# Performance work log

Hardware: AMD Instinct MI355X
Metric: run time of the kernel (lower is better)

## Reference

```python
import jax, jax.numpy as jnp
import numpy as np

B, N, C, H = 8, 1024, 1024, 16
D = C // H
SCALE = D ** -0.5


def setup_inputs() -> dict:
    key = jax.random.key(0)
    ks = jax.random.split(key, 5)
    s = 0.02  # keep pre-softmax logits in a sane range
    return {
        "x": jax.random.normal(ks[0], (B, N, C), dtype=jnp.float32),
        "Wq": jax.random.normal(ks[1], (C, C), dtype=jnp.float32) * s,
        "bq": jax.random.normal(ks[2], (C,), dtype=jnp.float32) * s,
        "Wkv": jax.random.normal(ks[3], (C, 2 * C), dtype=jnp.float32) * s,
        "bkv": jax.random.normal(ks[4], (2 * C,), dtype=jnp.float32) * s,
    }


def reference(x, Wq, bq, Wkv, bkv):
    b, n, c = x.shape
    h, d = H, c // H
    q = (x @ Wq + bq).reshape(b, n, h, d)                 # [b,n,h,d]
    kv = x @ Wkv + bkv                                     # [b,n,2c]
    k, v = jnp.split(kv, 2, axis=-1)                       # each [b,n,c]
    k = k.reshape(b, n, h, d)
    v = v.reshape(b, n, h, d)
    att = jnp.einsum("bnhd,bmhd->bnmh", q, k) * SCALE      # [b,n,m,h]
    att = jax.nn.softmax(att, axis=2)                      # softmax over keys (m)
    out = jnp.einsum("bnmh,bmhd->bnhd", att, v).reshape(b, n, c)
    return out
```

## Files before the change

kernel.cpp:

```cpp
#include <hip/hip_runtime.h>
#include <stdint.h>

using u16 = unsigned short;
using u32 = unsigned int;
using bf16x8 = __attribute__((ext_vector_type(8))) __bf16;
using f32x4  = __attribute__((ext_vector_type(4))) float;

#define NB 8
#define NN 1024
#define NC 1024
#define NH 16
#define ND 64
#define QSCALE 0.18033688011112042f

__device__ __forceinline__ u16 f2bf(float f) {
  u32 u = __float_as_uint(f);
  return (u16)((u + 0x7fffu + ((u >> 16) & 1u)) >> 16);
}
__device__ __forceinline__ u16 bfc(float f) {
  __bf16 b = (__bf16)f;
  return __builtin_bit_cast(u16, b);
}
__device__ __forceinline__ u32 pack2(u16 a, u16 b) { return (u32)a | ((u32)b << 16); }

__device__ __forceinline__ void gload16(const void* g, void* l) {
  __builtin_amdgcn_global_load_lds((__attribute__((address_space(1))) const u32*)g,
                                   (__attribute__((address_space(3))) u32*)l, 16, 0, 0);
}

__global__ void k_cvt_x(const float* __restrict__ x, u16* __restrict__ xb, int n4) {
  int i = blockIdx.x * blockDim.x + threadIdx.x;
  if (i >= n4) return;
  float4 v = ((const float4*)x)[i];
  ((uint2*)xb)[i] = make_uint2(pack2(f2bf(v.x), f2bf(v.y)), pack2(f2bf(v.z), f2bf(v.w)));
}

__global__ void k_prep_w(const float* __restrict__ Wq, const float* __restrict__ Wkv,
                         u16* __restrict__ Wt) {
  __shared__ u16 tile[64][72];
  int k0 = blockIdx.x * 64;
  int c0 = blockIdx.y * 64;
  int t  = threadIdx.x;
  bool isQ = (c0 < 1024);
  const float* src = isQ ? Wq : Wkv;
  int ldw  = isQ ? 1024 : 2048;
  int csrc = isQ ? c0 : (c0 - 1024);
  float sc = isQ ? QSCALE : 1.0f;

  int r  = t >> 2;
  int cq = (t & 3) << 4;
  const float* p = src + (size_t)(k0 + r) * ldw + csrc + cq;
#pragma unroll
  for (int j = 0; j < 16; j += 4) {
    float4 v = *(const float4*)(p + j);
    tile[r][cq + j + 0] = f2bf(v.x * sc);
    tile[r][cq + j + 1] = f2bf(v.y * sc);
    tile[r][cq + j + 2] = f2bf(v.z * sc);
    tile[r][cq + j + 3] = f2bf(v.w * sc);
  }
  __syncthreads();
  int co = t >> 2;
  int kq = (t & 3) << 4;
  u16 v0[16];
#pragma unroll
  for (int j = 0; j < 16; ++j) v0[j] = tile[kq + j][co];
  uint4 o0, o1;
  o0.x = pack2(v0[0], v0[1]);  o0.y = pack2(v0[2], v0[3]);
  o0.z = pack2(v0[4], v0[5]);  o0.w = pack2(v0[6], v0[7]);
  o1.x = pack2(v0[8], v0[9]);  o1.y = pack2(v0[10], v0[11]);
  o1.z = pack2(v0[12], v0[13]); o1.w = pack2(v0[14], v0[15]);
  u16* dst = Wt + (size_t)(c0 + co) * 1024 + k0 + kq;
  *(uint4*)dst = o0;
  *(uint4*)(dst + 8) = o1;
}

__global__ void k_bias(const float* __restrict__ bq, const float* __restrict__ bkv,
                       float* __restrict__ bias) {
  int i = blockIdx.x * 256 + threadIdx.x;
  if (i < 1024) bias[i] = bq[i] * QSCALE;
  else if (i < 3072) bias[i] = bkv[i - 1024];
}

__launch_bounds__(256)
__global__ void k_gemm(const u16* __restrict__ A, const u16* __restrict__ Bw,
                       const float* __restrict__ bias,
                       u16* __restrict__ qws, u16* __restrict__ kws, u16* __restrict__ vws) {
  __shared__ __align__(16) u16 As[128 * 32];
  __shared__ __align__(16) u16 Bs[128 * 32];
  int m0 = blockIdx.x * 128;
  int n0 = blockIdx.y * 128;
  int tid = threadIdx.x;
  int wave = tid >> 6, lane = tid & 63;
  int lo = lane & 15, hi = lane >> 4;
  int wr = wave >> 1, wc = wave & 1;

  f32x4 acc[4][4] = {};

  const u16* gA = A  + (size_t)(m0 + (wave * 2) * 16 + (lane >> 2)) * 1024 + (lane & 3) * 8;
  const u16* gB = Bw + (size_t)(n0 + (wave * 2) * 16 + (lane >> 2)) * 1024 + (lane & 3) * 8;
  u16* lA = As + (wave * 2) * 512;
  u16* lB = Bs + (wave * 2) * 512;

  for (int ko = 0; ko < 1024; ko += 32) {
    gload16(gA + ko,             lA);
    gload16(gA + ko + 16 * 1024, lA + 512);
    gload16(gB + ko,             lB);
    gload16(gB + ko + 16 * 1024, lB + 512);
    __syncthreads();
    bf16x8 af[4], bv[4];
#pragma unroll
    for (int mi = 0; mi < 4; ++mi)
      af[mi] = *(const bf16x8*)(As + (wr * 64 + mi * 16 + lo) * 32 + hi * 8);
#pragma unroll
    for (int ni = 0; ni < 4; ++ni)
      bv[ni] = *(const bf16x8*)(Bs + (wc * 64 + ni * 16 + lo) * 32 + hi * 8);
#pragma unroll
    for (int mi = 0; mi < 4; ++mi)
#pragma unroll
      for (int ni = 0; ni < 4; ++ni)
        acc[mi][ni] = __builtin_amdgcn_mfma_f32_16x16x32_bf16(af[mi], bv[ni], acc[mi][ni], 0, 0, 0);
    __syncthreads();
  }

#pragma unroll
  for (int ni = 0; ni < 4; ++ni) {
    int c = n0 + wc * 64 + ni * 16 + lo;
    float bvl = bias[c];
#pragma unroll
    for (int mi = 0; mi < 4; ++mi) {
#pragma unroll
      for (int r = 0; r < 4; ++r) {
        int m = m0 + wr * 64 + mi * 16 + hi * 4 + r;
        int b = m >> 10, tok = m & 1023;
        u16 o = f2bf(acc[mi][ni][r] + bvl);
        if (c < 1024) {
          int h = c >> 6, d = c & 63;
          qws[((size_t)(b * 16 + h) * 1024 + tok) * 64 + d] = o;
        } else if (c < 2048) {
          int c2 = c - 1024; int h = c2 >> 6, d = c2 & 63;
          kws[((size_t)(b * 16 + h) * 1024 + tok) * 64 + d] = o;
        } else {
          int c2 = c - 2048; int h = c2 >> 6, d = c2 & 63;
          vws[((size_t)(b * 16 + h) * 1024 + tok) * 64 + d] = o;
        }
      }
    }
  }
}

__global__ void k_tr_v(const u16* __restrict__ v, u16* __restrict__ vt) {
  __shared__ u16 t[64][72];
  int n0 = blockIdx.x * 64;
  int bh = blockIdx.y;
  int tid = threadIdx.x;
  const u16* src = v + ((size_t)bh * 1024 + n0) * 64;
#pragma unroll
  for (int p = 0; p < 2; ++p) {
    int r = p * 32 + (tid >> 3);
    int c = (tid & 7) * 8;
    *(uint4*)&t[r][c] = *(const uint4*)(src + r * 64 + c);
  }
  __syncthreads();
  int d = tid >> 2;
  int nq = (tid & 3) * 16;
  u16 v0[16];
#pragma unroll
  for (int j = 0; j < 16; ++j) v0[j] = t[nq + j][d];
  uint4 o0, o1;
  o0.x = pack2(v0[0], v0[1]);  o0.y = pack2(v0[2], v0[3]);
  o0.z = pack2(v0[4], v0[5]);  o0.w = pack2(v0[6], v0[7]);
  o1.x = pack2(v0[8], v0[9]);  o1.y = pack2(v0[10], v0[11]);
  o1.z = pack2(v0[12], v0[13]); o1.w = pack2(v0[14], v0[15]);
  u16* dst = vt + ((size_t)bh * 64 + d) * 1024 + n0 + nq;
  *(uint4*)dst = o0;
  *(uint4*)(dst + 8) = o1;
}

__launch_bounds__(512)
__global__ void k_attn(const u16* __restrict__ q, const u16* __restrict__ k,
                       const u16* __restrict__ vt, float* __restrict__ out) {
  __shared__ __align__(16) u16 Ks[2][4096];
  __shared__ __align__(16) u16 Vs[2][4096];
  __shared__ __align__(16) u16 P[8][16][72];
  int bh = blockIdx.x;
  int q0 = blockIdx.y * 128;
  int tid = threadIdx.x;
  int w = tid >> 6, lane = tid & 63;
  int lo = lane & 15, hi = lane >> 4;
  int b = bh >> 4, h = bh & 15;

  const u16* kbase = k  + (size_t)bh * 65536;
  const u16* vbase = vt + (size_t)bh * 65536;

  int srow = w * 8 + (lane >> 3);
  int cg   = (lane & 7) ^ ((lane >> 3) & 7);
  const u16* gK = kbase + (size_t)srow * 64   + cg * 8;
  const u16* gV = vbase + (size_t)srow * 1024 + cg * 8;
  u16* lK0 = &Ks[0][w * 512];
  u16* lK1 = &Ks[1][w * 512];
  u16* lV0 = &Vs[0][w * 512];
  u16* lV1 = &Vs[1][w * 512];

  const u16* qp = q + ((size_t)bh * 1024 + q0 + w * 16 + lo) * 64 + hi * 8;
  bf16x8 qf0 = *(const bf16x8*)(qp);
  bf16x8 qf1 = *(const bf16x8*)(qp + 32);

  f32x4 acc_o[4] = {};
  float m_s = -1e30f;
  float l_s = 0.f;

  int sw = lo & 7;

  gload16(gK, lK0);
  gload16(gV, lV0);
  __syncthreads();

  for (int t = 0; t < 16; ++t) {
    int cur = t & 1;
    if (t < 15) {
      gload16(gK + (t + 1) * 4096, cur ? lK0 : lK1);
      gload16(gV + (t + 1) * 64,   cur ? lV0 : lV1);
    }
    f32x4 s[4] = {};
    const u16* kb = Ks[cur];
#pragma unroll
    for (int ni = 0; ni < 4; ++ni) {
      const u16* kp = kb + (ni * 16 + lo) * 64;
      bf16x8 kf0 = *(const bf16x8*)(kp + ((hi ^ sw) * 8));
      bf16x8 kf1 = *(const bf16x8*)(kp + (((4 + hi) ^ sw) * 8));
      s[ni] = __builtin_amdgcn_mfma_f32_16x16x32_bf16(kf0, qf0, s[ni], 0, 0, 0);
      s[ni] = __builtin_amdgcn_mfma_f32_16x16x32_bf16(kf1, qf1, s[ni], 0, 0, 0);
    }
    float pm;
    {
      float a0 = fmaxf(fmaxf(s[0][0], s[0][1]), fmaxf(s[0][2], s[0][3]));
      float a1 = fmaxf(fmaxf(s[1][0], s[1][1]), fmaxf(s[1][2], s[1][3]));
      float a2 = fmaxf(fmaxf(s[2][0], s[2][1]), fmaxf(s[2][2], s[2][3]));
      float a3 = fmaxf(fmaxf(s[3][0], s[3][1]), fmaxf(s[3][2], s[3][3]));
      pm = fmaxf(fmaxf(a0, a1), fmaxf(a2, a3));
      pm = fmaxf(pm, __shfl_xor(pm, 16));
      pm = fmaxf(pm, __shfl_xor(pm, 32));
    }
    if (!__all(pm <= m_s + 8.0f)) {
      float mn = fmaxf(m_s, pm);
      float corr = __builtin_amdgcn_exp2f(m_s - mn);
      m_s = mn;
      l_s *= corr;
      float cr[4];
#pragma unroll
      for (int r = 0; r < 4; ++r) cr[r] = __shfl(corr, hi * 4 + r);
#pragma unroll
      for (int ci = 0; ci < 4; ++ci)
#pragma unroll
        for (int r = 0; r < 4; ++r) acc_o[ci][r] *= cr[r];
    }
    float rs = 0.f;
#pragma unroll
    for (int ni = 0; ni < 4; ++ni) {
      float p0 = __builtin_amdgcn_exp2f(s[ni][0] - m_s);
      float p1 = __builtin_amdgcn_exp2f(s[ni][1] - m_s);
      float p2 = __builtin_amdgcn_exp2f(s[ni][2] - m_s);
      float p3 = __builtin_amdgcn_exp2f(s[ni][3] - m_s);
      rs += (p0 + p1) + (p2 + p3);
      ushort4 pk;
      pk.x = bfc(p0); pk.y = bfc(p1); pk.z = bfc(p2); pk.w = bfc(p3);
      *(ushort4*)&P[w][lo][ni * 16 + hi * 4] = pk;
    }
    rs += __shfl_xor(rs, 16);
    rs += __shfl_xor(rs, 32);
    l_s += rs;
    bf16x8 pf0 = *(const bf16x8*)(&P[w][lo][hi * 8]);
    bf16x8 pf1 = *(const bf16x8*)(&P[w][lo][32 + hi * 8]);
    const u16* vb = Vs[cur];
#pragma unroll
    for (int ci = 0; ci < 4; ++ci) {
      const u16* vp = vb + (ci * 16 + lo) * 64;
      bf16x8 vf0 = *(const bf16x8*)(vp + ((hi ^ sw) * 8));
      bf16x8 vf1 = *(const bf16x8*)(vp + (((4 + hi) ^ sw) * 8));
      acc_o[ci] = __builtin_amdgcn_mfma_f32_16x16x32_bf16(pf0, vf0, acc_o[ci], 0, 0, 0);
      acc_o[ci] = __builtin_amdgcn_mfma_f32_16x16x32_bf16(pf1, vf1, acc_o[ci], 0, 0, 0);
    }
    __syncthreads();
  }
  float inv = 1.0f / l_s;
  float ivr[4];
#pragma unroll
  for (int r = 0; r < 4; ++r) ivr[r] = __shfl(inv, hi * 4 + r);
#pragma unroll
  for (int r = 0; r < 4; ++r) {
    int n = q0 + w * 16 + hi * 4 + r;
    float* dst = out + ((size_t)(b * 1024 + n)) * 1024 + h * 64;
#pragma unroll
    for (int ci = 0; ci < 4; ++ci) dst[ci * 16 + lo] = acc_o[ci][r] * ivr[r];
  }
}

extern "C" void kernel_launch(void* const* d_in, const int* in_sizes, int n_in,
                              void* d_out, int out_size, void* d_ws, size_t ws_size,
                              hipStream_t stream) {
  const float* x   = (const float*)d_in[0];
  const float* Wq  = (const float*)d_in[1];
  const float* bq  = (const float*)d_in[2];
  const float* Wkv = (const float*)d_in[3];
  const float* bkv = (const float*)d_in[4];
  float* out = (float*)d_out;

  char* ws = (char*)d_ws;
  u16*   xb   = (u16*)(ws);
  u16*   Wt   = (u16*)(ws + 16777216);
  float* bias = (float*)(ws + 23068672);
  u16*   qws  = (u16*)(ws + 23080960);
  u16*   kws  = (u16*)(ws + 39858176);
  u16*   vws  = (u16*)(ws + 56635392);
  u16*   vtw  = (u16*)(ws + 73412608);

  k_cvt_x<<<8192, 256, 0, stream>>>(x, xb, 2097152);
  {
    dim3 g(16, 48);
    k_prep_w<<<g, 256, 0, stream>>>(Wq, Wkv, Wt);
  }
  k_bias<<<12, 256, 0, stream>>>(bq, bkv, bias);
  {
    dim3 g(64, 24);
    k_gemm<<<g, 256, 0, stream>>>(xb, Wt, bias, qws, kws, vws);
  }
  {
    dim3 g(16, 128);
    k_tr_v<<<g, 256, 0, stream>>>(vws, vtw);
  }
  {
    dim3 g(128, 8);
    k_attn<<<g, 512, 0, stream>>>(qws, kws, vtw, out);
  }
}
```

Baseline: 148.9 us.

## Rewrite projection GEMM with 256x256 tiles, double-buffered swizzled LDS and interleaved prefetch

The QKV projection GEMM moves from 128x128 tiles with 4 waves and a single LDS buffer to 256x256 tiles with 8 waves, BK=64, and double-buffered LDS. The LDS layout is XOR-swizzled to avoid bank conflicts, and the global loads for the next k-step are split and interleaved between MFMA quadrants, with barriers and setprio to overlap memory and compute. The goals are higher arithmetic intensity per block and hidden load latency. In exchange it uses 128KB of LDS per block and a large accumulator register footprint, and the grid drops to 384 blocks, which may leave CUs underfilled.

```diff
diff --git a/kernel.cpp b/kernel.cpp
--- a/kernel.cpp
+++ b/kernel.cpp
@@ -81,58 +81,117 @@
   else if (i < 3072) bias[i] = bkv[i - 1024];
 }
 
-__launch_bounds__(256)
+__launch_bounds__(512, 2)
 __global__ void k_gemm(const u16* __restrict__ A, const u16* __restrict__ Bw,
                        const float* __restrict__ bias,
                        u16* __restrict__ qws, u16* __restrict__ kws, u16* __restrict__ vws) {
-  __shared__ __align__(16) u16 As[128 * 32];
-  __shared__ __align__(16) u16 Bs[128 * 32];
-  int m0 = blockIdx.x * 128;
-  int n0 = blockIdx.y * 128;
+  __shared__ __align__(16) u16 Ab[2][16384];
+  __shared__ __align__(16) u16 Bb[2][16384];
+  int m0 = blockIdx.x * 256;
+  int n0 = blockIdx.y * 256;
   int tid = threadIdx.x;
-  int wave = tid >> 6, lane = tid & 63;
+  int w = tid >> 6, lane = tid & 63;
   int lo = lane & 15, hi = lane >> 4;
-  int wr = wave >> 1, wc = wave & 1;
-
-  f32x4 acc[4][4] = {};
-
-  const u16* gA = A  + (size_t)(m0 + (wave * 2) * 16 + (lane >> 2)) * 1024 + (lane & 3) * 8;
-  const u16* gB = Bw + (size_t)(n0 + (wave * 2) * 16 + (lane >> 2)) * 1024 + (lane & 3) * 8;
-  u16* lA = As + (wave * 2) * 512;
-  u16* lB = Bs + (wave * 2) * 512;
-
-  for (int ko = 0; ko < 1024; ko += 32) {
-    gload16(gA + ko,             lA);
-    gload16(gA + ko + 16 * 1024, lA + 512);
-    gload16(gB + ko,             lB);
-    gload16(gB + ko + 16 * 1024, lB + 512);
-    __syncthreads();
-    bf16x8 af[4], bv[4];
-#pragma unroll
-    for (int mi = 0; mi < 4; ++mi)
-      af[mi] = *(const bf16x8*)(As + (wr * 64 + mi * 16 + lo) * 32 + hi * 8);
-#pragma unroll
-    for (int ni = 0; ni < 4; ++ni)
-      bv[ni] = *(const bf16x8*)(Bs + (wc * 64 + ni * 16 + lo) * 32 + hi * 8);
-#pragma unroll
-    for (int mi = 0; mi < 4; ++mi)
-#pragma unroll
-      for (int ni = 0; ni < 4; ++ni)
-        acc[mi][ni] = __builtin_amdgcn_mfma_f32_16x16x32_bf16(af[mi], bv[ni], acc[mi][ni], 0, 0, 0);
-    __syncthreads();
-  }
-
-#pragma unroll
-  for (int ni = 0; ni < 4; ++ni) {
-    int c = n0 + wc * 64 + ni * 16 + lo;
+  int wm = w >> 2, wn = w & 3;
+
+  f32x4 acc[8][4] = {};
+
+  int srow8 = lane >> 3;
+  int cs = (lane & 7) ^ srow8;
+  const u16* Ag = A  + (size_t)(m0 + w * 16 + srow8) * 1024 + cs * 8;
+  const u16* Bg = Bw + (size_t)(n0 + w * 16 + srow8) * 1024 + cs * 8;
+  int w2 = w * 2;
+
+  int sw = lo & 7;
+  int ck0 = ((hi) ^ sw) * 8;
+  int ck1 = ((4 + hi) ^ sw) * 8;
+  int arow = wm * 128 + lo;
+  int brow = wn * 64 + lo;
+
+#define STAGE4(gp, lp)                                        \
+  gload16((gp),                (lp) + w2 * 512);              \
+  gload16((gp) + 8 * 1024,     (lp) + (w2 + 1) * 512);        \
+  gload16((gp) + 128 * 1024,   (lp) + 8192 + w2 * 512);       \
+  gload16((gp) + 136 * 1024,   (lp) + 8192 + (w2 + 1) * 512);
+
+#define BARRIER() __builtin_amdgcn_s_barrier(); __builtin_amdgcn_sched_barrier(0)
+
+#define QUAD(AH, NH, AF)                                                          \
+  __builtin_amdgcn_s_setprio(1);                                                  \
+  _Pragma("unroll")                                                               \
+  for (int ks = 0; ks < 2; ++ks)                                                  \
+    _Pragma("unroll")                                                             \
+    for (int mi = 0; mi < 4; ++mi)                                                \
+      _Pragma("unroll")                                                           \
+      for (int ni = 0; ni < 2; ++ni)                                              \
+        acc[(AH) * 4 + mi][(NH) * 2 + ni] = __builtin_amdgcn_mfma_f32_16x16x32_bf16( \
+            AF[mi][ks], bf[NH][ni][ks], acc[(AH) * 4 + mi][(NH) * 2 + ni], 0, 0, 0); \
+  __builtin_amdgcn_s_setprio(0);
+
+  STAGE4(Ag, Ab[0]);
+  STAGE4(Bg, Bb[0]);
+  asm volatile("s_waitcnt vmcnt(0)" ::: "memory");
+  BARRIER();
+
+  for (int t = 0; t < 16; ++t) {
+    const u16* Acur = Ab[t & 1];
+    const u16* Bcur = Bb[t & 1];
+    u16* An = Ab[(t & 1) ^ 1];
+    u16* Bn = Bb[(t & 1) ^ 1];
+    int kn = (t + 1) * 64;
+    bool pre = (t < 15);
+
+    bf16x8 a0f[4][2], a1f[4][2], bf[2][2][2];
+#pragma unroll
+    for (int mi = 0; mi < 4; ++mi) {
+      const u16* p = Acur + (arow + mi * 16) * 64;
+      a0f[mi][0] = *(const bf16x8*)(p + ck0);
+      a0f[mi][1] = *(const bf16x8*)(p + ck1);
+    }
+#pragma unroll
+    for (int nh = 0; nh < 2; ++nh)
+#pragma unroll
+      for (int ni = 0; ni < 2; ++ni) {
+        const u16* p = Bcur + (brow + nh * 32 + ni * 16) * 64;
+        bf[nh][ni][0] = *(const bf16x8*)(p + ck0);
+        bf[nh][ni][1] = *(const bf16x8*)(p + ck1);
+      }
+    if (pre) { STAGE4(Ag + kn, An); }
+    BARRIER();
+    QUAD(0, 0, a0f);
+    BARRIER();
+    if (pre) { STAGE4(Bg + kn, Bn); }
+    BARRIER();
+    QUAD(0, 1, a0f);
+    BARRIER();
+#pragma unroll
+    for (int mi = 0; mi < 4; ++mi) {
+      const u16* p = Acur + (arow + 64 + mi * 16) * 64;
+      a1f[mi][0] = *(const bf16x8*)(p + ck0);
+      a1f[mi][1] = *(const bf16x8*)(p + ck1);
+    }
+    BARRIER();
+    QUAD(1, 0, a1f);
+    BARRIER();
+    QUAD(1, 1, a1f);
+    asm volatile("s_waitcnt vmcnt(0)" ::: "memory");
+    BARRIER();
+  }
+#undef STAGE4
+#undef BARRIER
+#undef QUAD
+
+#pragma unroll
+  for (int ni4 = 0; ni4 < 4; ++ni4) {
+    int c = n0 + wn * 64 + ni4 * 16 + lo;
     float bvl = bias[c];
 #pragma unroll
-    for (int mi = 0; mi < 4; ++mi) {
+    for (int mi8 = 0; mi8 < 8; ++mi8) {
 #pragma unroll
       for (int r = 0; r < 4; ++r) {
-        int m = m0 + wr * 64 + mi * 16 + hi * 4 + r;
+        int m = m0 + wm * 128 + mi8 * 16 + hi * 4 + r;
         int b = m >> 10, tok = m & 1023;
-        u16 o = f2bf(acc[mi][ni][r] + bvl);
+        u16 o = f2bf(acc[mi8][ni4][r] + bvl);
         if (c < 1024) {
           int h = c >> 6, d = c & 63;
           qws[((size_t)(b * 16 + h) * 1024 + tok) * 64 + d] = o;
@@ -321,8 +380,8 @@
   }
   k_bias<<<12, 256, 0, stream>>>(bq, bkv, bias);
   {
-    dim3 g(64, 24);
-    k_gemm<<<g, 256, 0, stream>>>(xb, Wt, bias, qws, kws, vws);
+    dim3 g(32, 12);
+    k_gemm<<<g, 512, 0, stream>>>(xb, Wt, bias, qws, kws, vws);
   }
   {
     dim3 g(16, 128);
```

Result: no change. 148.5 us (-0.3%).

## Enlarge QKV GEMM tiles and add 4-stage async LDS pipeline with swizzle

Applied to the files above, without the earlier changes.

The projection GEMM moves from 128x128 tiles with 256 threads to 256x256 tiles with 512 threads. It adds a four-buffer LDS ring where global-to-LDS loads run two stages ahead, using vmcnt waits with a single barrier per k-step instead of two. The LDS layout is XOR-swizzled to avoid bank conflicts. This targets the load-latency stalls and sync overhead of the single-buffered loop, at the cost of 128KB of LDS, more accumulator registers and only 384 blocks across the grid.

```diff
diff --git a/kernel.cpp b/kernel.cpp
--- a/kernel.cpp
+++ b/kernel.cpp
@@ -81,56 +81,86 @@
   else if (i < 3072) bias[i] = bkv[i - 1024];
 }
 
-__launch_bounds__(256)
+__launch_bounds__(512, 2)
 __global__ void k_gemm(const u16* __restrict__ A, const u16* __restrict__ Bw,
                        const float* __restrict__ bias,
                        u16* __restrict__ qws, u16* __restrict__ kws, u16* __restrict__ vws) {
-  __shared__ __align__(16) u16 As[128 * 32];
-  __shared__ __align__(16) u16 Bs[128 * 32];
-  int m0 = blockIdx.x * 128;
-  int n0 = blockIdx.y * 128;
+  __shared__ __align__(16) u16 RA[4][8192];
+  __shared__ __align__(16) u16 RB[4][8192];
+  int m0 = blockIdx.x * 256;
+  int n0 = blockIdx.y * 256;
   int tid = threadIdx.x;
-  int wave = tid >> 6, lane = tid & 63;
+  int w = tid >> 6, lane = tid & 63;
   int lo = lane & 15, hi = lane >> 4;
-  int wr = wave >> 1, wc = wave & 1;
-
-  f32x4 acc[4][4] = {};
-
-  const u16* gA = A  + (size_t)(m0 + (wave * 2) * 16 + (lane >> 2)) * 1024 + (lane & 3) * 8;
-  const u16* gB = Bw + (size_t)(n0 + (wave * 2) * 16 + (lane >> 2)) * 1024 + (lane & 3) * 8;
-  u16* lA = As + (wave * 2) * 512;
-  u16* lB = Bs + (wave * 2) * 512;
-
-  for (int ko = 0; ko < 1024; ko += 32) {
-    gload16(gA + ko,             lA);
-    gload16(gA + ko + 16 * 1024, lA + 512);
-    gload16(gB + ko,             lB);
-    gload16(gB + ko + 16 * 1024, lB + 512);
-    __syncthreads();
-    bf16x8 af[4], bv[4];
-#pragma unroll
-    for (int mi = 0; mi < 4; ++mi)
-      af[mi] = *(const bf16x8*)(As + (wr * 64 + mi * 16 + lo) * 32 + hi * 8);
-#pragma unroll
-    for (int ni = 0; ni < 4; ++ni)
-      bv[ni] = *(const bf16x8*)(Bs + (wc * 64 + ni * 16 + lo) * 32 + hi * 8);
-#pragma unroll
-    for (int mi = 0; mi < 4; ++mi)
-#pragma unroll
-      for (int ni = 0; ni < 4; ++ni)
-        acc[mi][ni] = __builtin_amdgcn_mfma_f32_16x16x32_bf16(af[mi], bv[ni], acc[mi][ni], 0, 0, 0);
-    __syncthreads();
-  }
+  int wm = w >> 2, wn = w & 3;
+
+  f32x4 acc[8][4] = {};
+
+  int srow = w * 16 + (lane >> 2);
+  int csw  = ((lane & 3) ^ ((lane >> 3) & 3)) * 8;
+  const u16* Ag = A  + (size_t)(m0 + srow) * 1024 + csw;
+  const u16* Bg = Bw + (size_t)(n0 + srow) * 1024 + csw;
+  int ldsoff = w * 512;
+
+  int ck = ((hi ^ ((lo >> 1) & 3)) << 3);
+  int arow = (wm * 128 + lo) * 32;
+  int brow = (wn * 64 + lo) * 32;
+
+#define STAGEU(U)                                                   \
+  {                                                                 \
+    int _s = (U) & 3;                                               \
+    const u16* _ag = Ag + (U) * 32;                                 \
+    const u16* _bg = Bg + (U) * 32;                                 \
+    gload16(_ag,              &RA[_s][ldsoff]);                     \
+    gload16(_ag + 128 * 1024, &RA[_s][4096 + ldsoff]);              \
+    gload16(_bg,              &RB[_s][ldsoff]);                     \
+    gload16(_bg + 128 * 1024, &RB[_s][4096 + ldsoff]);              \
+  }
+
+#define COMPUTEU(U)                                                 \
+  {                                                                 \
+    int _s = (U) & 3;                                               \
+    bf16x8 af[8], bfr[4];                                           \
+    _Pragma("unroll")                                               \
+    for (int mi = 0; mi < 8; ++mi)                                  \
+      af[mi] = *(const bf16x8*)(&RA[_s][arow + mi * 512 + ck]);     \
+    _Pragma("unroll")                                               \
+    for (int ni = 0; ni < 4; ++ni)                                  \
+      bfr[ni] = *(const bf16x8*)(&RB[_s][brow + ni * 512 + ck]);    \
+    _Pragma("unroll")                                               \
+    for (int mi = 0; mi < 8; ++mi)                                  \
+      _Pragma("unroll")                                             \
+      for (int ni = 0; ni < 4; ++ni)                                \
+        acc[mi][ni] = __builtin_amdgcn_mfma_f32_16x16x32_bf16(      \
+            af[mi], bfr[ni], acc[mi][ni], 0, 0, 0);                 \
+  }
+
+  STAGEU(0);
+  STAGEU(1);
+  for (int u = 0; u < 30; ++u) {
+    STAGEU(u + 2);
+    asm volatile("s_waitcnt vmcnt(8)" ::: "memory");
+    __builtin_amdgcn_s_barrier();
+    COMPUTEU(u);
+  }
+  asm volatile("s_waitcnt vmcnt(4)" ::: "memory");
+  __builtin_amdgcn_s_barrier();
+  COMPUTEU(30);
+  asm volatile("s_waitcnt vmcnt(0)" ::: "memory");
+  __builtin_amdgcn_s_barrier();
+  COMPUTEU(31);
+#undef STAGEU
+#undef COMPUTEU
 
 #pragma unroll
   for (int ni = 0; ni < 4; ++ni) {
-    int c = n0 + wc * 64 + ni * 16 + lo;
+    int c = n0 + wn * 64 + ni * 16 + lo;
     float bvl = bias[c];
 #pragma unroll
-    for (int mi = 0; mi < 4; ++mi) {
+    for (int mi = 0; mi < 8; ++mi) {
 #pragma unroll
       for (int r = 0; r < 4; ++r) {
-        int m = m0 + wr * 64 + mi * 16 + hi * 4 + r;
+        int m = m0 + wm * 128 + mi * 16 + hi * 4 + r;
         int b = m >> 10, tok = m & 1023;
         u16 o = f2bf(acc[mi][ni][r] + bvl);
         if (c < 1024) {
@@ -321,8 +351,8 @@
   }
   k_bias<<<12, 256, 0, stream>>>(bq, bkv, bias);
   {
-    dim3 g(64, 24);
-    k_gemm<<<g, 256, 0, stream>>>(xb, Wt, bias, qws, kws, vws);
+    dim3 g(32, 12);
+    k_gemm<<<g, 512, 0, stream>>>(xb, Wt, bias, qws, kws, vws);
   }
   {
     dim3 g(16, 128);
```

Measured after the change: 144.6 us. 1.03x faster.

## Merge prep kernels, fuse V transpose into double-buffered swizzled GEMM epilogue

Applied to the files above, without the earlier changes.

Merges the x-conversion, weight-transpose and bias kernels into one launch. The QKV GEMM now uses 512 threads with a 128x256 tile, double-buffered LDS staging with an XOR swizzle, and an L2-friendly block remap. V is written straight out in transposed layout from the GEMM epilogue, which removes the separate transpose kernel and the intermediate V buffer. The trade-offs are more LDS per block and strided 8-byte transposed stores for V.

```diff
diff --git a/kernel.cpp b/kernel.cpp
--- a/kernel.cpp
+++ b/kernel.cpp
@@ -28,152 +28,151 @@
                                    (__attribute__((address_space(3))) u32*)l, 16, 0, 0);
 }
 
-__global__ void k_cvt_x(const float* __restrict__ x, u16* __restrict__ xb, int n4) {
-  int i = blockIdx.x * blockDim.x + threadIdx.x;
-  if (i >= n4) return;
-  float4 v = ((const float4*)x)[i];
-  ((uint2*)xb)[i] = make_uint2(pack2(f2bf(v.x), f2bf(v.y)), pack2(f2bf(v.z), f2bf(v.w)));
-}
-
-__global__ void k_prep_w(const float* __restrict__ Wq, const float* __restrict__ Wkv,
-                         u16* __restrict__ Wt) {
+__global__ void k_prep(const float* __restrict__ x, const float* __restrict__ Wq,
+                       const float* __restrict__ bq, const float* __restrict__ Wkv,
+                       const float* __restrict__ bkv,
+                       u16* __restrict__ xb, u16* __restrict__ Wt, float* __restrict__ bias) {
   __shared__ u16 tile[64][72];
-  int k0 = blockIdx.x * 64;
-  int c0 = blockIdx.y * 64;
-  int t  = threadIdx.x;
-  bool isQ = (c0 < 1024);
-  const float* src = isQ ? Wq : Wkv;
-  int ldw  = isQ ? 1024 : 2048;
-  int csrc = isQ ? c0 : (c0 - 1024);
-  float sc = isQ ? QSCALE : 1.0f;
-
-  int r  = t >> 2;
-  int cq = (t & 3) << 4;
-  const float* p = src + (size_t)(k0 + r) * ldw + csrc + cq;
-#pragma unroll
-  for (int j = 0; j < 16; j += 4) {
-    float4 v = *(const float4*)(p + j);
-    tile[r][cq + j + 0] = f2bf(v.x * sc);
-    tile[r][cq + j + 1] = f2bf(v.y * sc);
-    tile[r][cq + j + 2] = f2bf(v.z * sc);
-    tile[r][cq + j + 3] = f2bf(v.w * sc);
-  }
-  __syncthreads();
-  int co = t >> 2;
-  int kq = (t & 3) << 4;
-  u16 v0[16];
-#pragma unroll
-  for (int j = 0; j < 16; ++j) v0[j] = tile[kq + j][co];
-  uint4 o0, o1;
-  o0.x = pack2(v0[0], v0[1]);  o0.y = pack2(v0[2], v0[3]);
-  o0.z = pack2(v0[4], v0[5]);  o0.w = pack2(v0[6], v0[7]);
-  o1.x = pack2(v0[8], v0[9]);  o1.y = pack2(v0[10], v0[11]);
-  o1.z = pack2(v0[12], v0[13]); o1.w = pack2(v0[14], v0[15]);
-  u16* dst = Wt + (size_t)(c0 + co) * 1024 + k0 + kq;
-  *(uint4*)dst = o0;
-  *(uint4*)(dst + 8) = o1;
-}
-
-__global__ void k_bias(const float* __restrict__ bq, const float* __restrict__ bkv,
-                       float* __restrict__ bias) {
-  int i = blockIdx.x * 256 + threadIdx.x;
-  if (i < 1024) bias[i] = bq[i] * QSCALE;
-  else if (i < 3072) bias[i] = bkv[i - 1024];
-}
-
-__launch_bounds__(256)
+  int bid = blockIdx.x;
+  int t = threadIdx.x;
+  if (bid < 8192) {
+    int i = bid * 256 + t;
+    float4 v = ((const float4*)x)[i];
+    ((uint2*)xb)[i] = make_uint2(pack2(f2bf(v.x), f2bf(v.y)), pack2(f2bf(v.z), f2bf(v.w)));
+    return;
+  }
+  if (bid < 8960) {
+    int pb = bid - 8192;
+    int k0 = (pb & 15) << 6;
+    int c0 = (pb >> 4) << 6;
+    bool isQ = (c0 < 1024);
+    const float* src = isQ ? Wq : Wkv;
+    int ldw  = isQ ? 1024 : 2048;
+    int csrc = isQ ? c0 : (c0 - 1024);
+    float sc = isQ ? QSCALE : 1.0f;
+
+    int r  = t >> 2;
+    int cq = (t & 3) << 4;
+    const float* p = src + (size_t)(k0 + r) * ldw + csrc + cq;
+#pragma unroll
+    for (int j = 0; j < 16; j += 4) {
+      float4 v = *(const float4*)(p + j);
+      tile[r][cq + j + 0] = f2bf(v.x * sc);
+      tile[r][cq + j + 1] = f2bf(v.y * sc);
+      tile[r][cq + j + 2] = f2bf(v.z * sc);
+      tile[r][cq + j + 3] = f2bf(v.w * sc);
+    }
+    __syncthreads();
+    int co = t >> 2;
+    int kq = (t & 3) << 4;
+    u16 v0[16];
+#pragma unroll
+    for (int j = 0; j < 16; ++j) v0[j] = tile[kq + j][co];
+    uint4 o0, o1;
+    o0.x = pack2(v0[0], v0[1]);  o0.y = pack2(v0[2], v0[3]);
+    o0.z = pack2(v0[4], v0[5]);  o0.w = pack2(v0[6], v0[7]);
+    o1.x = pack2(v0[8], v0[9]);  o1.y = pack2(v0[10], v0[11]);
+    o1.z = pack2(v0[12], v0[13]); o1.w = pack2(v0[14], v0[15]);
+    u16* dst = Wt + (size_t)(c0 + co) * 1024 + k0 + kq;
+    *(uint4*)dst = o0;
+    *(uint4*)(dst + 8) = o1;
+    return;
+  }
+  {
+    int i = (bid - 8960) * 256 + t;
+    if (i < 1024) bias[i] = bq[i] * QSCALE;
+    else if (i < 3072) bias[i] = bkv[i - 1024];
+  }
+}
+
+__launch_bounds__(512, 4)
 __global__ void k_gemm(const u16* __restrict__ A, const u16* __restrict__ Bw,
                        const float* __restrict__ bias,
-                       u16* __restrict__ qws, u16* __restrict__ kws, u16* __restrict__ vws) {
-  __shared__ __align__(16) u16 As[128 * 32];
-  __shared__ __align__(16) u16 Bs[128 * 32];
-  int m0 = blockIdx.x * 128;
-  int n0 = blockIdx.y * 128;
+                       u16* __restrict__ qws, u16* __restrict__ kws, u16* __restrict__ vtw) {
+  __shared__ __align__(16) u16 Ab[2][4096];
+  __shared__ __align__(16) u16 Bb[2][8192];
+  int flat = blockIdx.x;
+  int swz = (flat & 7) * 96 + (flat >> 3);
+  int m0 = (swz & 63) * 128;
+  int n0 = (swz >> 6) * 256;
   int tid = threadIdx.x;
-  int wave = tid >> 6, lane = tid & 63;
+  int w = tid >> 6, lane = tid & 63;
   int lo = lane & 15, hi = lane >> 4;
-  int wr = wave >> 1, wc = wave & 1;
+  int wm = w >> 2, wn = w & 3;
 
   f32x4 acc[4][4] = {};
 
-  const u16* gA = A  + (size_t)(m0 + (wave * 2) * 16 + (lane >> 2)) * 1024 + (lane & 3) * 8;
-  const u16* gB = Bw + (size_t)(n0 + (wave * 2) * 16 + (lane >> 2)) * 1024 + (lane & 3) * 8;
-  u16* lA = As + (wave * 2) * 512;
-  u16* lB = Bs + (wave * 2) * 512;
-
-  for (int ko = 0; ko < 1024; ko += 32) {
-    gload16(gA + ko,             lA);
-    gload16(gA + ko + 16 * 1024, lA + 512);
-    gload16(gB + ko,             lB);
-    gload16(gB + ko + 16 * 1024, lB + 512);
+  int srow = tid >> 2;
+  int schunk = (tid & 3) ^ ((tid >> 3) & 3);
+  const u16* Ag  = A  + (size_t)(m0 + srow) * 1024 + schunk * 8;
+  const u16* Bg0 = Bw + (size_t)(n0 + srow) * 1024 + schunk * 8;
+  const u16* Bg1 = Bw + (size_t)(n0 + 128 + srow) * 1024 + schunk * 8;
+
+  int ck = ((hi ^ ((lo >> 1) & 3)) << 3);
+
+#define STAGE(BUF, KO)                                  \
+  gload16(Ag  + (KO), &Ab[BUF][tid * 8]);               \
+  gload16(Bg0 + (KO), &Bb[BUF][tid * 8]);               \
+  gload16(Bg1 + (KO), &Bb[BUF][4096 + tid * 8]);
+
+  STAGE(0, 0);
+  __syncthreads();
+
+  for (int t = 0; t < 32; ++t) {
+    int cb = t & 1;
+    if (t < 31) { STAGE(cb ^ 1, (t + 1) * 32); }
+    bf16x8 af[4], bfr[4];
+#pragma unroll
+    for (int mi = 0; mi < 4; ++mi)
+      af[mi] = *(const bf16x8*)&Ab[cb][(wm * 64 + mi * 16 + lo) * 32 + ck];
+#pragma unroll
+    for (int ni = 0; ni < 4; ++ni)
+      bfr[ni] = *(const bf16x8*)&Bb[cb][(wn * 64 + ni * 16 + lo) * 32 + ck];
+#pragma unroll
+    for (int mi = 0; mi < 4; ++mi)
+#pragma unroll
+      for (int ni = 0; ni < 4; ++ni)
+        acc[mi][ni] = __builtin_amdgcn_mfma_f32_16x16x32_bf16(af[mi], bfr[ni], acc[mi][ni], 0, 0, 0);
     __syncthreads();
-    bf16x8 af[4], bv[4];
-#pragma unroll
-    for (int mi = 0; mi < 4; ++mi)
-      af[mi] = *(const bf16x8*)(As + (wr * 64 + mi * 16 + lo) * 32 + hi * 8);
-#pragma unroll
-    for (int ni = 0; ni < 4; ++ni)
-      bv[ni] = *(const bf16x8*)(Bs + (wc * 64 + ni * 16 + lo) * 32 + hi * 8);
-#pragma unroll
-    for (int mi = 0; mi < 4; ++mi)
-#pragma unroll
-      for (int ni = 0; ni < 4; ++ni)
-        acc[mi][ni] = __builtin_amdgcn_mfma_f32_16x16x32_bf16(af[mi], bv[ni], acc[mi][ni], 0, 0, 0);
-    __syncthreads();
-  }
+  }
+#undef STAGE
 
 #pragma unroll
   for (int ni = 0; ni < 4; ++ni) {
-    int c = n0 + wc * 64 + ni * 16 + lo;
+    int c = n0 + wn * 64 + ni * 16 + lo;
     float bvl = bias[c];
-#pragma unroll
-    for (int mi = 0; mi < 4; ++mi) {
-#pragma unroll
-      for (int r = 0; r < 4; ++r) {
-        int m = m0 + wr * 64 + mi * 16 + hi * 4 + r;
-        int b = m >> 10, tok = m & 1023;
-        u16 o = f2bf(acc[mi][ni][r] + bvl);
-        if (c < 1024) {
-          int h = c >> 6, d = c & 63;
-          qws[((size_t)(b * 16 + h) * 1024 + tok) * 64 + d] = o;
-        } else if (c < 2048) {
-          int c2 = c - 1024; int h = c2 >> 6, d = c2 & 63;
-          kws[((size_t)(b * 16 + h) * 1024 + tok) * 64 + d] = o;
-        } else {
-          int c2 = c - 2048; int h = c2 >> 6, d = c2 & 63;
-          vws[((size_t)(b * 16 + h) * 1024 + tok) * 64 + d] = o;
+    if (c < 2048) {
+#pragma unroll
+      for (int mi = 0; mi < 4; ++mi) {
+#pragma unroll
+        for (int r = 0; r < 4; ++r) {
+          int m = m0 + wm * 64 + mi * 16 + hi * 4 + r;
+          int b = m >> 10, tok = m & 1023;
+          u16 o = f2bf(acc[mi][ni][r] + bvl);
+          if (c < 1024) {
+            int h = c >> 6, d = c & 63;
+            qws[((size_t)(b * 16 + h) * 1024 + tok) * 64 + d] = o;
+          } else {
+            int c2 = c - 1024; int h = c2 >> 6, d = c2 & 63;
+            kws[((size_t)(b * 16 + h) * 1024 + tok) * 64 + d] = o;
+          }
         }
       }
-    }
-  }
-}
-
-__global__ void k_tr_v(const u16* __restrict__ v, u16* __restrict__ vt) {
-  __shared__ u16 t[64][72];
-  int n0 = blockIdx.x * 64;
-  int bh = blockIdx.y;
-  int tid = threadIdx.x;
-  const u16* src = v + ((size_t)bh * 1024 + n0) * 64;
-#pragma unroll
-  for (int p = 0; p < 2; ++p) {
-    int r = p * 32 + (tid >> 3);
-    int c = (tid & 7) * 8;
-    *(uint4*)&t[r][c] = *(const uint4*)(src + r * 64 + c);
-  }
-  __syncthreads();
-  int d = tid >> 2;
-  int nq = (tid & 3) * 16;
-  u16 v0[16];
-#pragma unroll
-  for (int j = 0; j < 16; ++j) v0[j] = t[nq + j][d];
-  uint4 o0, o1;
-  o0.x = pack2(v0[0], v0[1]);  o0.y = pack2(v0[2], v0[3]);
-  o0.z = pack2(v0[4], v0[5]);  o0.w = pack2(v0[6], v0[7]);
-  o1.x = pack2(v0[8], v0[9]);  o1.y = pack2(v0[10], v0[11]);
-  o1.z = pack2(v0[12], v0[13]); o1.w = pack2(v0[14], v0[15]);
-  u16* dst = vt + ((size_t)bh * 64 + d) * 1024 + n0 + nq;
-  *(uint4*)dst = o0;
-  *(uint4*)(dst + 8) = o1;
+    } else {
+      int c2 = c - 2048; int h = c2 >> 6, d = c2 & 63;
+#pragma unroll
+      for (int mi = 0; mi < 4; ++mi) {
+        int m = m0 + wm * 64 + mi * 16 + hi * 4;
+        int b = m >> 10, tok = m & 1023;
+        ushort4 pk;
+        pk.x = bfc(acc[mi][ni][0] + bvl);
+        pk.y = bfc(acc[mi][ni][1] + bvl);
+        pk.z = bfc(acc[mi][ni][2] + bvl);
+        pk.w = bfc(acc[mi][ni][3] + bvl);
+        *(ushort4*)&vtw[((size_t)(b * 16 + h) * 64 + d) * 1024 + tok] = pk;
+      }
+    }
+  }
 }
 
 __launch_bounds__(512)
@@ -311,23 +310,10 @@
   float* bias = (float*)(ws + 23068672);
   u16*   qws  = (u16*)(ws + 23080960);
   u16*   kws  = (u16*)(ws + 39858176);
-  u16*   vws  = (u16*)(ws + 56635392);
   u16*   vtw  = (u16*)(ws + 73412608);
 
-  k_cvt_x<<<8192, 256, 0, stream>>>(x, xb, 2097152);
-  {
-    dim3 g(16, 48);
-    k_prep_w<<<g, 256, 0, stream>>>(Wq, Wkv, Wt);
-  }
-  k_bias<<<12, 256, 0, stream>>>(bq, bkv, bias);
-  {
-    dim3 g(64, 24);
-    k_gemm<<<g, 256, 0, stream>>>(xb, Wt, bias, qws, kws, vws);
-  }
-  {
-    dim3 g(16, 128);
-    k_tr_v<<<g, 256, 0, stream>>>(vws, vtw);
-  }
+  k_prep<<<8972, 256, 0, stream>>>(x, Wq, bq, Wkv, bkv, xb, Wt, bias);
+  k_gemm<<<768, 512, 0, stream>>>(xb, Wt, bias, qws, kws, vtw);
   {
     dim3 g(128, 8);
     k_attn<<<g, 512, 0, stream>>>(qws, kws, vtw, out);
```

Measured after the change: 139.4 us. -6.4%, faster.
